# Kernel optimization log

Hardware: AMD Instinct MI355X
Metric: run time of the kernel (lower is better)

The kernel has to match this reference:

```python
import jax, jax.numpy as jnp
import numpy as np

NEG_SLOPE = 0.2


def setup_inputs() -> dict:
    key = jax.random.key(0)
    ks = jax.random.split(key, 12)
    N, D = 50000, 256
    H, C = 4, 128          # heads, per-head channels; H*C = gnn_hidden_dim = 512
    E = 800000
    edge_index = jax.random.randint(ks[0], (2, E), 0, N, dtype=jnp.int64)
    edge_weight = jax.random.uniform(ks[1], (E,), dtype=jnp.float32)
    s = 1.0 / np.sqrt(D)
    return {
        'edge_index': edge_index,
        'edge_weight': edge_weight,
        'emb':     jax.random.normal(ks[2], (N, D), jnp.float32),
        'W':       jax.random.normal(ks[3], (D, H * C), jnp.float32) * s,
        'att_src': jax.random.normal(ks[4], (H, C), jnp.float32) * s,
        'att_dst': jax.random.normal(ks[5], (H, C), jnp.float32) * s,
        'att_edge': jax.random.normal(ks[6], (H, C), jnp.float32) * s,
        'W_edge':  jax.random.normal(ks[7], (1, H * C), jnp.float32),
        'bias':    jnp.zeros((H * C,), jnp.float32),
        'W_out':   jax.random.normal(ks[8], (H * C, D), jnp.float32) * s,
        'b_out':   jnp.zeros((D,), jnp.float32),
    }


def reference(edge_index, edge_weight, emb, W, att_src, att_dst, att_edge,
              W_edge, bias, W_out, b_out):
    N, D = emb.shape
    H, C = att_src.shape
    src, dst = edge_index[0], edge_index[1]
    E = src.shape[0]

    # GATConv: shared linear projection for src and dst (in_channels is int)
    x = (emb @ W).reshape(N, H, C)                     # [N,H,C]

    # add self loops; edge_attr for loops = per-dst mean of incoming edge_attr
    ones = jnp.ones((E,), emb.dtype)
    cnt = jax.ops.segment_sum(ones, dst, num_segments=N)
    ea_mean = jax.ops.segment_sum(edge_weight, dst, num_segments=N) / jnp.maximum(cnt, 1.0)
    loop = jnp.arange(N, dtype=src.dtype)
    src_f = jnp.concatenate([src, loop])
    dst_f = jnp.concatenate([dst, loop])
    ea = jnp.concatenate([edge_weight, ea_mean])[:, None]   # [E+N, 1]

    e_feat = (ea @ W_edge).reshape(-1, H, C)            # [E+N,H,C]

    a_src = jnp.einsum('nhc,hc->nh', x, att_src)        # [N,H]
    a_dst = jnp.einsum('nhc,hc->nh', x, att_dst)
    a_e = jnp.einsum('ehc,hc->eh', e_feat, att_edge)    # [E+N,H]

    alpha = jax.nn.leaky_relu(a_src[src_f] + a_dst[dst_f] + a_e, NEG_SLOPE)
    # segment softmax over destination neighborhoods
    m = jax.ops.segment_max(alpha, dst_f, num_segments=N)
    alpha = jnp.exp(alpha - m[dst_f])
    denom = jax.ops.segment_sum(alpha, dst_f, num_segments=N)
    alpha = alpha / (denom[dst_f] + 1e-16)              # [E+N,H]

    msg = x[src_f] * alpha[..., None]                   # [E+N,H,C]
    out = jax.ops.segment_sum(msg, dst_f, num_segments=N).reshape(N, H * C) + bias

    return out @ W_out + b_out                          # [N,D]
```

## Files before the change

kernel.cpp:

```cpp
#include <hip/hip_runtime.h>
#include <cstdint>
#include <cstddef>

#define NEG_SLOPE 0.2f
#define HC 512
#define NH 4
#define CAP 64

typedef __attribute__((ext_vector_type(8))) short bf16x8;
typedef __attribute__((ext_vector_type(4))) float f32x4;

__device__ inline float lrelu(float z) { return z > 0.f ? z : NEG_SLOPE * z; }

__device__ inline unsigned short f2bf(float f) {
    unsigned u = __float_as_uint(f);
    u += 0x7FFFu + ((u >> 16) & 1u);
    return (unsigned short)(u >> 16);
}
__device__ inline float bflo(unsigned v) { return __uint_as_float(v << 16); }
__device__ inline float bfhi(unsigned v) { return __uint_as_float(v & 0xffff0000u); }

#define GLOAD16(gp, lp) \
    __builtin_amdgcn_global_load_lds( \
        (const __attribute__((address_space(1))) unsigned int*)(const void*)(gp), \
        (__attribute__((address_space(3))) unsigned int*)(void*)(lp), 16, 0, 0)

__global__ __launch_bounds__(256) void prep00_kernel(
        const float* __restrict__ W, const float* __restrict__ W_out,
        const float* __restrict__ att_s, const float* __restrict__ att_d,
        const float* __restrict__ W_edge, const float* __restrict__ att_edge,
        const float* __restrict__ bias, const float* __restrict__ b_out,
        float* __restrict__ watt, float* __restrict__ bc4, float* __restrict__ sh,
        uint4* __restrict__ zptr, int zcount) {
    int b = blockIdx.x, t = threadIdx.x;
    if (b < 8) {
        int h = b & 3;
        const float* att = (b < 4) ? att_s : att_d;
        float s = 0.f;
        for (int c = 0; c < 128; ++c)
            s += W[(size_t)t * HC + h * 128 + c] * att[h * 128 + c];
        watt[b * 256 + t] = s;
    } else if (b < 12) {
        int part = b - 8;
        int j0 = part * 128;
        float s = (part == 0) ? b_out[t] : 0.f;
        for (int j = j0; j < j0 + 128; ++j)
            s += bias[j] * W_out[(size_t)j * 256 + t];
        bc4[part * 256 + t] = s;
    } else if (b == 12) {
        if (t < NH) {
            float s = 0.f;
            for (int c = 0; c < 128; ++c)
                s += W_edge[t * 128 + c] * att_edge[t * 128 + c];
            sh[t] = s;
        }
    } else {
        int idx = (b - 13) * 256 + t;
        if (idx < zcount) zptr[idx] = (uint4){0u, 0u, 0u, 0u};
    }
}

__global__ __launch_bounds__(256) void mega1_kernel(
        const int* __restrict__ ei, const float* __restrict__ ew, int E,
        int* __restrict__ cnt, int2* __restrict__ csr2,
        const float* __restrict__ W, const float* __restrict__ W_out,
        unsigned short* __restrict__ Wb, unsigned short* __restrict__ WoT,
        const float4* __restrict__ embf4, const float* __restrict__ watt,
        uint2* __restrict__ embq, float* __restrict__ a_src,
        float* __restrict__ a_dst, int N, int nEmb) {
    int b = blockIdx.x, t = threadIdx.x;
    int r6 = b % 6, q6 = b / 6;

    if (r6 == 0) {
        int lane = t & 63;
        unsigned long long nzm = __ballot(ei[2 * lane + 1] != 0);
        int is64 = (nzm == 0ull) ? 1 : 0;
        int base = q6 * 1024;

        int dv[4], sv[4];
        float wv[4];
        bool ok[4];
        #pragma unroll
        for (int r = 0; r < 4; ++r) {
            int e = base + r * 256 + t;
            ok[r] = (e < E);
            if (ok[r]) {
                size_t de = (size_t)E + e;
                dv[r] = is64 ? ei[2 * de] : ei[de];
                sv[r] = is64 ? ei[2 * (size_t)e] : ei[e];
                wv[r] = ew[e];
            }
        }
        int pos[4];
        #pragma unroll
        for (int r = 0; r < 4; ++r)
            if (ok[r]) pos[r] = atomicAdd(&cnt[dv[r]], 1);
        #pragma unroll
        for (int r = 0; r < 4; ++r)
            if (ok[r] && pos[r] < CAP)
                csr2[(size_t)dv[r] * CAP + pos[r]] =
                    make_int2(sv[r], __float_as_int(wv[r]));
        return;
    }

    int aux = q6 * 5 + r6 - 1;
    if (aux < 128) {
        int i = aux * 256 + t;
        float4 v = reinterpret_cast<const float4*>(W)[i];
        ushort4 o;
        o.x = f2bf(v.x); o.y = f2bf(v.y); o.z = f2bf(v.z); o.w = f2bf(v.w);
        reinterpret_cast<ushort4*>(Wb)[i] = o;
    } else if (aux < 640) {
        int idx = (aux - 128) * 256 + t;
        int r = idx >> 8, c = idx & 255;
        WoT[(size_t)c * 512 + r] = f2bf(W_out[idx]);
    } else if (aux < 640 + nEmb) {
        int bb = aux - 640;
        int wid = t >> 6, lane = t & 63;
        #pragma unroll
        for (int j = 0; j < 4; ++j) {
            int n = bb * 16 + wid * 4 + j;
            if (n >= N) break;
            float4 v = embf4[(size_t)n * 64 + lane];
            uint2 o;
            o.x = (unsigned)f2bf(v.x) | ((unsigned)f2bf(v.y) << 16);
            o.y = (unsigned)f2bf(v.z) | ((unsigned)f2bf(v.w) << 16);
            embq[(size_t)n * 64 + lane] = o;
            float r[8];
            #pragma unroll
            for (int i = 0; i < 8; ++i) {
                float4 wv = reinterpret_cast<const float4*>(watt)[i * 64 + lane];
                r[i] = v.x * wv.x + v.y * wv.y + v.z * wv.z + v.w * wv.w;
            }
            #pragma unroll
            for (int off = 32; off > 0; off >>= 1) {
                #pragma unroll
                for (int i = 0; i < 8; ++i) r[i] += __shfl_xor(r[i], off);
            }
            if (lane == 0) {
                size_t bofs = (size_t)n * 4;
                a_src[bofs + 0] = r[0]; a_src[bofs + 1] = r[1];
                a_src[bofs + 2] = r[2]; a_src[bofs + 3] = r[3];
                a_dst[bofs + 0] = r[4]; a_dst[bofs + 1] = r[5];
                a_dst[bofs + 2] = r[6]; a_dst[bofs + 3] = r[7];
            }
        }
    }
}

__global__ __launch_bounds__(256) void mt_kernel(
        const unsigned short* __restrict__ WoT, const unsigned short* __restrict__ Wb,
        unsigned short* __restrict__ MT) {
    __shared__ __align__(16) unsigned short As[128 * 64];
    __shared__ __align__(16) unsigned short Bs[128 * 64];
    int b = blockIdx.x, t = threadIdx.x;
    int lane = t & 63, w = t >> 6;
    int bn = (b & 1) * 128, bm = ((b >> 1) & 1) * 128, z = b >> 2;
    const unsigned short* A  = WoT + (size_t)z * 128;
    const unsigned short* BT = Wb  + (size_t)z * 128;
    int wr = w >> 1, wc = w & 1;

    f32x4 acc[4][4];
    #pragma unroll
    for (int i = 0; i < 4; ++i)
        #pragma unroll
        for (int j = 0; j < 4; ++j)
            acc[i][j] = (f32x4){0.f, 0.f, 0.f, 0.f};

    int lr = lane & 15, kb = lane >> 4;
    int q = lane & 7;

    for (int k0 = 0; k0 < 128; k0 += 64) {
        #pragma unroll
        for (int p = 0; p < 4; ++p) {
            int row = p * 32 + w * 8 + (lane >> 3);
            int ce  = ((q ^ (row & 7)) << 3) + k0;
            int ob  = p * 4096 + w * 1024;
            GLOAD16(A  + (size_t)(bm + row) * 512 + ce, (char*)As + ob);
            GLOAD16(BT + (size_t)(bn + row) * 512 + ce, (char*)Bs + ob);
        }
        __syncthreads();
        #pragma unroll
        for (int kk = 0; kk < 2; ++kk) {
            bf16x8 a[4], bfr[4];
            #pragma unroll
            for (int i = 0; i < 4; ++i) {
                int row = wr * 64 + i * 16 + lr;
                a[i] = *reinterpret_cast<const bf16x8*>(
                    &As[row * 64 + (((kk * 4 + kb) ^ (row & 7)) << 3)]);
            }
            #pragma unroll
            for (int j = 0; j < 4; ++j) {
                int row = wc * 64 + j * 16 + lr;
                bfr[j] = *reinterpret_cast<const bf16x8*>(
                    &Bs[row * 64 + (((kk * 4 + kb) ^ (row & 7)) << 3)]);
            }
            #pragma unroll
            for (int i = 0; i < 4; ++i)
                #pragma unroll
                for (int j = 0; j < 4; ++j)
                    acc[i][j] = __builtin_amdgcn_mfma_f32_16x16x32_bf16(a[i], bfr[j], acc[i][j], 0, 0, 0);
        }
        __syncthreads();
    }
    int rg = lane >> 4;
    #pragma unroll
    for (int i = 0; i < 4; ++i)
        #pragma unroll
        for (int r = 0; r < 4; ++r) {
            int row = bm + wr * 64 + i * 16 + rg * 4 + r;
            #pragma unroll
            for (int j = 0; j < 4; ++j) {
                int col = bn + wc * 64 + j * 16 + lr;
                MT[(size_t)row * 1024 + z * 256 + col] = f2bf(acc[i][j][r]);
            }
        }
}

#define EFMA(W_, V_) { \
    float e0_ = bflo(V_.x), e1_ = bfhi(V_.x), e2_ = bflo(V_.y), e3_ = bfhi(V_.y); \
    a00 += W_.x * e0_; a01 += W_.x * e1_; a02 += W_.x * e2_; a03 += W_.x * e3_; \
    a10 += W_.y * e0_; a11 += W_.y * e1_; a12 += W_.y * e2_; a13 += W_.y * e3_; \
    a20 += W_.z * e0_; a21 += W_.z * e1_; a22 += W_.z * e2_; a23 += W_.z * e3_; \
    a30 += W_.w * e0_; a31 += W_.w * e1_; a32 += W_.w * e2_; a33 += W_.w * e3_; \
    den0 += W_.x; den1 += W_.y; den2 += W_.z; den3 += W_.w; }

__global__ __launch_bounds__(256) void agg_kernel(
        const uint2* __restrict__ embq, const float* __restrict__ a_src,
        const float* __restrict__ a_dst, const int* __restrict__ cnt,
        const float* __restrict__ sh, const int2* __restrict__ csr2,
        uint2* __restrict__ aggn, int N) {
    int wid = threadIdx.x >> 6, lane = threadIdx.x & 63;
    int n = blockIdx.x * 4 + wid;
    if (n >= N) return;
    int deg = cnt[n];
    int m = deg < CAP ? deg : CAP;

    __shared__ int s_src[4][64];
    __shared__ __align__(16) float s_alpha[4][64][4];

    int k1 = 0x7FFFFFFF, k2 = 0x7FFFFFFF;
    if (lane < m) {
        int2 p = csr2[(size_t)n * CAP + lane];
        k1 = p.x; k2 = p.y;
    }
    #pragma unroll
    for (int k = 2; k <= 64; k <<= 1) {
        #pragma unroll
        for (int j = k >> 1; j > 0; j >>= 1) {
            int o1 = __shfl_xor(k1, j);
            int o2 = __shfl_xor(k2, j);
            bool lower = (lane & j) == 0;
            bool asc = (lane & k) == 0;
            bool cmp = (k1 > o1) || (k1 == o1 && k2 > o2);
            if ((cmp == lower) == asc) { k1 = o1; k2 = o2; }
        }
    }
    float wgt = (lane < m) ? __int_as_float(k2) : 0.f;

    float wsl = wgt;
    #pragma unroll
    for (int o = 32; o > 0; o >>= 1) wsl += __shfl_xor(wsl, o);
    float eam = wsl / fmaxf((float)deg, 1.f);

    float ad0 = a_dst[(size_t)n * 4 + 0], ad1 = a_dst[(size_t)n * 4 + 1];
    float ad2 = a_dst[(size_t)n * 4 + 2], ad3 = a_dst[(size_t)n * 4 + 3];
    float sh0 = sh[0], sh1 = sh[1], sh2 = sh[2], sh3 = sh[3];
    float es0 = __expf(lrelu(a_src[(size_t)n * 4 + 0] + ad0 + eam * sh0));
    float es1 = __expf(lrelu(a_src[(size_t)n * 4 + 1] + ad1 + eam * sh1));
    float es2 = __expf(lrelu(a_src[(size_t)n * 4 + 2] + ad2 + eam * sh2));
    float es3 = __expf(lrelu(a_src[(size_t)n * 4 + 3] + ad3 + eam * sh3));

    uint2 xv = embq[(size_t)n * 64 + lane];
    float d0 = bflo(xv.x), d1 = bfhi(xv.x), d2 = bflo(xv.y), d3 = bfhi(xv.y);

    float a00 = es0 * d0, a01 = es0 * d1, a02 = es0 * d2, a03 = es0 * d3;
    float a10 = es1 * d0, a11 = es1 * d1, a12 = es1 * d2, a13 = es1 * d3;
    float a20 = es2 * d0, a21 = es2 * d1, a22 = es2 * d2, a23 = es2 * d3;
    float a30 = es3 * d0, a31 = es3 * d1, a32 = es3 * d2, a33 = es3 * d3;
    float den0 = es0, den1 = es1, den2 = es2, den3 = es3;

    if (lane < m) {
        int s = k1;
        s_src[wid][lane] = s;
        float4 as4 = *reinterpret_cast<const float4*>(&a_src[(size_t)s * 4]);
        s_alpha[wid][lane][0] = __expf(lrelu(as4.x + ad0 + wgt * sh0));
        s_alpha[wid][lane][1] = __expf(lrelu(as4.y + ad1 + wgt * sh1));
        s_alpha[wid][lane][2] = __expf(lrelu(as4.z + ad2 + wgt * sh2));
        s_alpha[wid][lane][3] = __expf(lrelu(as4.w + ad3 + wgt * sh3));
    }
    int e2 = 0;
    for (; e2 + 2 <= m; e2 += 2) {
        int s0 = s_src[wid][e2], s1 = s_src[wid][e2 + 1];
        float4 w0 = *reinterpret_cast<const float4*>(s_alpha[wid][e2]);
        float4 w1 = *reinterpret_cast<const float4*>(s_alpha[wid][e2 + 1]);
        uint2 v0 = embq[(size_t)s0 * 64 + lane];
        uint2 v1 = embq[(size_t)s1 * 64 + lane];
        EFMA(w0, v0); EFMA(w1, v1);
    }
    if (e2 < m) {
        int s0 = s_src[wid][e2];
        float4 w0 = *reinterpret_cast<const float4*>(s_alpha[wid][e2]);
        uint2 v0 = embq[(size_t)s0 * 64 + lane];
        EFMA(w0, v0);
    }

    float i0 = 1.f / (den0 + 1e-16f), i1 = 1.f / (den1 + 1e-16f);
    float i2 = 1.f / (den2 + 1e-16f), i3 = 1.f / (den3 + 1e-16f);
    size_t base = (size_t)n * 256 + lane;
    uint2 o;
    o.x = (unsigned)f2bf(a00 * i0) | ((unsigned)f2bf(a01 * i0) << 16);
    o.y = (unsigned)f2bf(a02 * i0) | ((unsigned)f2bf(a03 * i0) << 16);
    aggn[base] = o;
    o.x = (unsigned)f2bf(a10 * i1) | ((unsigned)f2bf(a11 * i1) << 16);
    o.y = (unsigned)f2bf(a12 * i1) | ((unsigned)f2bf(a13 * i1) << 16);
    aggn[base + 64] = o;
    o.x = (unsigned)f2bf(a20 * i2) | ((unsigned)f2bf(a21 * i2) << 16);
    o.y = (unsigned)f2bf(a22 * i2) | ((unsigned)f2bf(a23 * i2) << 16);
    aggn[base + 128] = o;
    o.x = (unsigned)f2bf(a30 * i3) | ((unsigned)f2bf(a31 * i3) << 16);
    o.y = (unsigned)f2bf(a32 * i3) | ((unsigned)f2bf(a33 * i3) << 16);
    aggn[base + 192] = o;
}

__global__ __launch_bounds__(512) void gemm_out_kernel(
        const unsigned short* __restrict__ A,
        const unsigned short* __restrict__ BT,
        const float* __restrict__ bc4, float* __restrict__ C, int M) {
    __shared__ __align__(16) unsigned short As[128 * 64];
    __shared__ __align__(16) unsigned short Bs[256 * 64];
    int tid = threadIdx.x;
    int lane = tid & 63, w = tid >> 6;
    int bm = blockIdx.x * 128;
    int wr = w >> 2, wc = w & 3;

    f32x4 acc[4][4];
    #pragma unroll
    for (int i = 0; i < 4; ++i)
        #pragma unroll
        for (int j = 0; j < 4; ++j)
            acc[i][j] = (f32x4){0.f, 0.f, 0.f, 0.f};

    int lr = lane & 15, kb = lane >> 4;
    int q = lane & 7;

    for (int k0 = 0; k0 < 1024; k0 += 64) {
        #pragma unroll
        for (int p = 0; p < 2; ++p) {
            int row = p * 64 + w * 8 + (lane >> 3);
            int ce  = ((q ^ (row & 7)) << 3) + k0;
            int ob  = p * 8192 + w * 1024;
            int gr = bm + row; if (gr >= M) gr = M - 1;
            GLOAD16(A + (size_t)gr * 1024 + ce, (char*)As + ob);
        }
        #pragma unroll
        for (int p = 0; p < 4; ++p) {
            int row = p * 64 + w * 8 + (lane >> 3);
            int ce  = ((q ^ (row & 7)) << 3) + k0;
            int ob  = p * 8192 + w * 1024;
            GLOAD16(BT + (size_t)row * 1024 + ce, (char*)Bs + ob);
        }
        __syncthreads();

        #pragma unroll
        for (int kk = 0; kk < 2; ++kk) {
            bf16x8 a[4], b[4];
            #pragma unroll
            for (int i = 0; i < 4; ++i) {
                int row = wr * 64 + i * 16 + lr;
                a[i] = *reinterpret_cast<const bf16x8*>(
                    &As[row * 64 + (((kk * 4 + kb) ^ (row & 7)) << 3)]);
            }
            #pragma unroll
            for (int j = 0; j < 4; ++j) {
                int row = wc * 64 + j * 16 + lr;
                b[j] = *reinterpret_cast<const bf16x8*>(
                    &Bs[row * 64 + (((kk * 4 + kb) ^ (row & 7)) << 3)]);
            }
            #pragma unroll
            for (int i = 0; i < 4; ++i)
                #pragma unroll
                for (int j = 0; j < 4; ++j)
                    acc[i][j] = __builtin_amdgcn_mfma_f32_16x16x32_bf16(a[i], b[j], acc[i][j], 0, 0, 0);
        }
        __syncthreads();
    }

    int rg = lane >> 4;
    #pragma unroll
    for (int i = 0; i < 4; ++i) {
        #pragma unroll
        for (int r = 0; r < 4; ++r) {
            int row = bm + wr * 64 + i * 16 + rg * 4 + r;
            if (row >= M) continue;
            #pragma unroll
            for (int j = 0; j < 4; ++j) {
                int col = wc * 64 + j * 16 + lr;
                float bval = bc4[col] + bc4[256 + col] + bc4[512 + col] + bc4[768 + col];
                C[(size_t)row * 256 + col] = acc[i][j][r] + bval;
            }
        }
    }
}

extern "C" void kernel_launch(void* const* d_in, const int* in_sizes, int n_in,
                              void* d_out, int out_size, void* d_ws, size_t ws_size,
                              hipStream_t stream) {
    const int*   edge_index  = (const int*)d_in[0];
    const float* edge_weight = (const float*)d_in[1];
    const float* emb         = (const float*)d_in[2];
    const float* W           = (const float*)d_in[3];
    const float* att_src     = (const float*)d_in[4];
    const float* att_dst     = (const float*)d_in[5];
    const float* att_edge    = (const float*)d_in[6];
    const float* W_edge      = (const float*)d_in[7];
    const float* bias        = (const float*)d_in[8];
    const float* W_out       = (const float*)d_in[9];
    const float* b_out       = (const float*)d_in[10];
    float* out = (float*)d_out;

    const int E = in_sizes[1];
    const int D = 256;
    const int N = in_sizes[2] / D;
    const int mb = (N + 127) / 128;
    const int nEmb = (N + 15) / 16;
    const int nEdge4 = (E + 1023) / 1024;

    char* ws = (char*)d_ws;
    size_t off = 0;
    auto alloc = [&](size_t bytes) {
        size_t o = off;
        off += (bytes + 255) & ~(size_t)255;
        return o;
    };
    unsigned short* embb  = (unsigned short*)(ws + alloc((size_t)N * D * 2));
    unsigned short* aggn  = (unsigned short*)(ws + alloc((size_t)N * 1024 * 2));
    unsigned short* Wb    = (unsigned short*)(ws + alloc((size_t)D * HC * 2));
    unsigned short* WoT   = (unsigned short*)(ws + alloc((size_t)HC * D * 2));
    unsigned short* MT    = (unsigned short*)(ws + alloc((size_t)256 * 1024 * 2));
    float* watt    = (float*)(ws + alloc(2048 * 4));
    float* bc4     = (float*)(ws + alloc(1024 * 4));
    float* a_src   = (float*)(ws + alloc((size_t)N * 4 * 4));
    float* a_dst   = (float*)(ws + alloc((size_t)N * 4 * 4));
    float* sh      = (float*)(ws + alloc(64));
    size_t zbytes  = ((size_t)N * 4 + 15) & ~(size_t)15;
    size_t zoff    = alloc(zbytes);
    int*   cnt     = (int*)(ws + zoff);
    int2*  csr2    = (int2*)(ws + alloc((size_t)N * CAP * 8));
    (void)ws_size; (void)n_in; (void)out_size;

    int zcount = (int)(zbytes / 16);
    int nz = (zcount + 255) / 256;

    prep00_kernel<<<13 + nz, 256, 0, stream>>>(
        W, W_out, att_src, att_dst, W_edge, att_edge, bias, b_out,
        watt, bc4, sh, (uint4*)(ws + zoff), zcount);

    mega1_kernel<<<nEdge4 * 6, 256, 0, stream>>>(
        edge_index, edge_weight, E, cnt, csr2,
        W, W_out, Wb, WoT,
        (const float4*)emb, watt, (uint2*)embb, a_src, a_dst, N, nEmb);

    mt_kernel<<<16, 256, 0, stream>>>(WoT, Wb, MT);

    agg_kernel<<<(N + 3) / 4, 256, 0, stream>>>(
        (const uint2*)embb, a_src, a_dst, cnt, sh, csr2, (uint2*)aggn, N);

    gemm_out_kernel<<<mb, 512, 0, stream>>>(aggn, MT, bc4, out, N);
}
```

Before: 226.0 us.

## Compute folded weight matrix MT inside mega1 with fp32 FMA, drop mt_kernel

Measured after the change: 227.3 us. No clear change (+0.6%).

```diff
diff --git a/kernel.cpp b/kernel.cpp
--- a/kernel.cpp
+++ b/kernel.cpp
@@ -64,10 +64,11 @@
         const int* __restrict__ ei, const float* __restrict__ ew, int E,
         int* __restrict__ cnt, int2* __restrict__ csr2,
         const float* __restrict__ W, const float* __restrict__ W_out,
-        unsigned short* __restrict__ Wb, unsigned short* __restrict__ WoT,
+        unsigned short* __restrict__ MT,
         const float4* __restrict__ embf4, const float* __restrict__ watt,
         uint2* __restrict__ embq, float* __restrict__ a_src,
         float* __restrict__ a_dst, int N, int nEmb) {
+    __shared__ float sW[512];
     int b = blockIdx.x, t = threadIdx.x;
     int r6 = b % 6, q6 = b / 6;
 
@@ -104,18 +105,21 @@
     }
 
     int aux = q6 * 5 + r6 - 1;
-    if (aux < 128) {
-        int i = aux * 256 + t;
-        float4 v = reinterpret_cast<const float4*>(W)[i];
-        ushort4 o;
-        o.x = f2bf(v.x); o.y = f2bf(v.y); o.z = f2bf(v.z); o.w = f2bf(v.w);
-        reinterpret_cast<ushort4*>(Wb)[i] = o;
-    } else if (aux < 640) {
-        int idx = (aux - 128) * 256 + t;
-        int r = idx >> 8, c = idx & 255;
-        WoT[(size_t)c * 512 + r] = f2bf(W_out[idx]);
-    } else if (aux < 640 + nEmb) {
-        int bb = aux - 640;
+    if (aux < 256) {
+        int j = aux;
+        sW[t] = W_out[(size_t)t * 256 + j];
+        sW[256 + t] = W_out[(size_t)(256 + t) * 256 + j];
+        __syncthreads();
+        const float* wrow = &W[(size_t)t * HC];
+        #pragma unroll
+        for (int h = 0; h < NH; ++h) {
+            float s = 0.f;
+            for (int c = 0; c < 128; ++c)
+                s += wrow[h * 128 + c] * sW[h * 128 + c];
+            MT[(size_t)j * 1024 + h * 256 + t] = f2bf(s);
+        }
+    } else if (aux < 256 + nEmb) {
+        int bb = aux - 256;
         int wid = t >> 6, lane = t & 63;
         #pragma unroll
         for (int j = 0; j < 4; ++j) {
@@ -146,75 +150,6 @@
             }
         }
     }
-}
-
-__global__ __launch_bounds__(256) void mt_kernel(
-        const unsigned short* __restrict__ WoT, const unsigned short* __restrict__ Wb,
-        unsigned short* __restrict__ MT) {
-    __shared__ __align__(16) unsigned short As[128 * 64];
-    __shared__ __align__(16) unsigned short Bs[128 * 64];
-    int b = blockIdx.x, t = threadIdx.x;
-    int lane = t & 63, w = t >> 6;
-    int bn = (b & 1) * 128, bm = ((b >> 1) & 1) * 128, z = b >> 2;
-    const unsigned short* A  = WoT + (size_t)z * 128;
-    const unsigned short* BT = Wb  + (size_t)z * 128;
-    int wr = w >> 1, wc = w & 1;
-
-    f32x4 acc[4][4];
-    #pragma unroll
-    for (int i = 0; i < 4; ++i)
-        #pragma unroll
-        for (int j = 0; j < 4; ++j)
-            acc[i][j] = (f32x4){0.f, 0.f, 0.f, 0.f};
-
-    int lr = lane & 15, kb = lane >> 4;
-    int q = lane & 7;
-
-    for (int k0 = 0; k0 < 128; k0 += 64) {
-        #pragma unroll
-        for (int p = 0; p < 4; ++p) {
-            int row = p * 32 + w * 8 + (lane >> 3);
-            int ce  = ((q ^ (row & 7)) << 3) + k0;
-            int ob  = p * 4096 + w * 1024;
-            GLOAD16(A  + (size_t)(bm + row) * 512 + ce, (char*)As + ob);
-            GLOAD16(BT + (size_t)(bn + row) * 512 + ce, (char*)Bs + ob);
-        }
-        __syncthreads();
-        #pragma unroll
-        for (int kk = 0; kk < 2; ++kk) {
-            bf16x8 a[4], bfr[4];
-            #pragma unroll
-            for (int i = 0; i < 4; ++i) {
-                int row = wr * 64 + i * 16 + lr;
-                a[i] = *reinterpret_cast<const bf16x8*>(
-                    &As[row * 64 + (((kk * 4 + kb) ^ (row & 7)) << 3)]);
-            }
-            #pragma unroll
-            for (int j = 0; j < 4; ++j) {
-                int row = wc * 64 + j * 16 + lr;
-                bfr[j] = *reinterpret_cast<const bf16x8*>(
-                    &Bs[row * 64 + (((kk * 4 + kb) ^ (row & 7)) << 3)]);
-            }
-            #pragma unroll
-            for (int i = 0; i < 4; ++i)
-                #pragma unroll
-                for (int j = 0; j < 4; ++j)
-                    acc[i][j] = __builtin_amdgcn_mfma_f32_16x16x32_bf16(a[i], bfr[j], acc[i][j], 0, 0, 0);
-        }
-        __syncthreads();
-    }
-    int rg = lane >> 4;
-    #pragma unroll
-    for (int i = 0; i < 4; ++i)
-        #pragma unroll
-        for (int r = 0; r < 4; ++r) {
-            int row = bm + wr * 64 + i * 16 + rg * 4 + r;
-            #pragma unroll
-            for (int j = 0; j < 4; ++j) {
-                int col = bn + wc * 64 + j * 16 + lr;
-                MT[(size_t)row * 1024 + z * 256 + col] = f2bf(acc[i][j][r]);
-            }
-        }
 }
 
 #define EFMA(W_, V_) { \
@@ -435,8 +370,6 @@
     };
     unsigned short* embb  = (unsigned short*)(ws + alloc((size_t)N * D * 2));
     unsigned short* aggn  = (unsigned short*)(ws + alloc((size_t)N * 1024 * 2));
-    unsigned short* Wb    = (unsigned short*)(ws + alloc((size_t)D * HC * 2));
-    unsigned short* WoT   = (unsigned short*)(ws + alloc((size_t)HC * D * 2));
     unsigned short* MT    = (unsigned short*)(ws + alloc((size_t)256 * 1024 * 2));
     float* watt    = (float*)(ws + alloc(2048 * 4));
     float* bc4     = (float*)(ws + alloc(1024 * 4));
@@ -458,10 +391,8 @@
 
     mega1_kernel<<<nEdge4 * 6, 256, 0, stream>>>(
         edge_index, edge_weight, E, cnt, csr2,
-        W, W_out, Wb, WoT,
+        W, W_out, MT,
         (const float4*)emb, watt, (uint2*)embb, a_src, a_dst, N, nEmb);
-
-    mt_kernel<<<16, 256, 0, stream>>>(WoT, Wb, MT);
 
     agg_kernel<<<(N + 3) / 4, 256, 0, stream>>>(
         (const uint2*)embb, a_src, a_dst, cnt, sh, csr2, (uint2*)aggn, N);
```
